# Performance work log

Measured on AMD Instinct MI355X. Metric: run time of the kernel, lower is better.

## Reference

```python
import jax, jax.numpy as jnp
import numpy as np

DIM = 96
HEADS = 6
WS = 8                      # window_size
OWS = int(WS * 0.5) + WS    # overlap_win_size = 12
PAD = (OWS - WS) // 2       # 2
Dd = Hh = Ww = 24
B = 1
L = Dd * Hh * Ww
MLP_H = DIM * 2
TBL = (WS + OWS - 1) ** 3   # 6859 relative-position-bias entries


def setup_inputs() -> dict:
    key = jax.random.key(0)
    ks = jax.random.split(key, 8)
    def n(k, shape, s=0.02):
        return jax.random.normal(k, shape, jnp.float32) * s
    return {
        "x": jax.random.normal(ks[0], (B, L, DIM), jnp.float32),
        "ln1_w": jnp.ones((DIM,), jnp.float32),
        "ln1_b": jnp.zeros((DIM,), jnp.float32),
        "qkv_w": n(ks[1], (3 * DIM, DIM)),
        "qkv_b": jnp.zeros((3 * DIM,), jnp.float32),
        "rpb": n(ks[2], (TBL, HEADS)),
        "proj_w": n(ks[3], (DIM, DIM)),
        "proj_b": jnp.zeros((DIM,), jnp.float32),
        "ln2_w": jnp.ones((DIM,), jnp.float32),
        "ln2_b": jnp.zeros((DIM,), jnp.float32),
        "fc1_w": n(ks[4], (MLP_H, DIM)),
        "fc1_b": jnp.zeros((MLP_H,), jnp.float32),
        "fc2_w": n(ks[5], (DIM, MLP_H)),
        "fc2_b": jnp.zeros((DIM,), jnp.float32),
        "rpi": jax.random.randint(ks[6], (WS ** 3, OWS ** 3), 0, TBL),
        "D": Dd, "H": Hh, "W": Ww,
    }


def _ln(x, w, b):
    m = jnp.mean(x, -1, keepdims=True)
    v = jnp.var(x, -1, keepdims=True)
    return (x - m) / jnp.sqrt(v + 1e-5) * w + b


def _ocab3d(x, ln1_w, ln1_b, qkv_w, qkv_b, rpb, proj_w, proj_b,
            ln2_w, ln2_b, fc1_w, fc1_b, fc2_w, fc2_b, rpi, D, H, W):
    Bz, Lz, C = x.shape
    hd = C // HEADS
    scale = hd ** -0.5
    shortcut = x

    xn = _ln(x, ln1_w, ln1_b).reshape(Bz, D, H, W, C)
    qkv = xn @ qkv_w.T + qkv_b                   # [B,D,H,W,3C]
    q = qkv[..., :C]
    kv = qkv[..., C:]                            # cat(k, v) on channels, [B,D,H,W,2C]

    nD, nH, nW = D // WS, H // WS, W // WS
    nw = nD * nH * nW

    # non-overlapping query windows -> [B*nw, WS^3, C]
    qw = q.reshape(Bz, nD, WS, nH, WS, nW, WS, C)
    qw = qw.transpose(0, 1, 3, 5, 2, 4, 6, 7).reshape(Bz * nw, WS ** 3, C)

    # overlapping kv windows via pad + strided gather (mirrors F.pad + unfold)
    kvp = jnp.pad(kv, ((0, 0), (PAD, PAD), (PAD, PAD), (PAD, PAD), (0, 0)))
    idx_d = (jnp.arange(nD) * WS)[:, None] + jnp.arange(OWS)[None, :]
    idx_h = (jnp.arange(nH) * WS)[:, None] + jnp.arange(OWS)[None, :]
    idx_w = (jnp.arange(nW) * WS)[:, None] + jnp.arange(OWS)[None, :]
    kw = kvp[:, idx_d]                 # [B,nD,OWS,Hp,Wp,2C]
    kw = kw[:, :, :, idx_h]            # [B,nD,OWS,nH,OWS,Wp,2C]
    kw = kw[:, :, :, :, :, idx_w]      # [B,nD,OWS,nH,OWS,nW,OWS,2C]
    kw = kw.transpose(0, 1, 3, 5, 2, 4, 6, 7).reshape(Bz * nw, OWS ** 3, 2 * C)
    kk, vv = kw[..., :C], kw[..., C:]

    qh = qw.reshape(-1, WS ** 3, HEADS, hd).transpose(0, 2, 1, 3) * scale
    kh = kk.reshape(-1, OWS ** 3, HEADS, hd).transpose(0, 2, 1, 3)
    vh = vv.reshape(-1, OWS ** 3, HEADS, hd).transpose(0, 2, 1, 3)

    attn = jnp.einsum('bhqd,bhkd->bhqk', qh, kh)               # [B*nw,H,512,1728]
    bias = rpb[rpi.reshape(-1)].reshape(WS ** 3, OWS ** 3, HEADS).transpose(2, 0, 1)
    attn = jax.nn.softmax(attn + bias[None], axis=-1)
    out = jnp.einsum('bhqk,bhkd->bhqd', attn, vh)
    out = out.transpose(0, 2, 1, 3).reshape(Bz * nw, WS ** 3, C)

    # window reverse -> [B, L, C]
    out = out.reshape(Bz, nD, nH, nW, WS, WS, WS, C)
    out = out.transpose(0, 1, 4, 2, 5, 3, 6, 7).reshape(Bz, D * H * W, C)

    x2 = out @ proj_w.T + proj_b + shortcut
    h1 = jax.nn.gelu(_ln(x2, ln2_w, ln2_b) @ fc1_w.T + fc1_b, approximate=False)
    return x2 + (h1 @ fc2_w.T + fc2_b)


def reference(x, ln1_w, ln1_b, qkv_w, qkv_b, rpb, proj_w, proj_b,
              ln2_w, ln2_b, fc1_w, fc1_b, fc2_w, fc2_b, rpi, D, H, W):
    return _ocab3d(x, ln1_w, ln1_b, qkv_w, qkv_b, rpb, proj_w, proj_b,
                   ln2_w, ln2_b, fc1_w, fc1_b, fc2_w, fc2_b, rpi, D, H, W)
```

## Files before the change

kernel.cpp:

```cpp
#include <hip/hip_runtime.h>
#include <math.h>

#define DIMC   96
#define NHEADS 6
#define HD     16
#define WSZ    8
#define OWSZ   12
#define PADW   2
#define DD     24
#define LTOK   13824
#define NWIN   27
#define NKEY   1728
#define NROW   512
#define MLPH   192
#define PDIM   28
#define PD3    21952
#define TBL    6859
#define LSTR   82944
#define AOSTR  1327104
#define LOG2E  1.4426950408889634f

typedef __attribute__((ext_vector_type(4))) short bf16x4;
typedef __attribute__((ext_vector_type(8))) short bf16x8;
typedef __attribute__((ext_vector_type(4))) float f32x4;

__device__ __forceinline__ unsigned short bfround(float f) {
    unsigned u = __float_as_uint(f);
    return (unsigned short)((u + 0x7FFFu + ((u >> 16) & 1u)) >> 16);
}
__device__ __forceinline__ unsigned bfpack(float a, float b) {
    unsigned ua = __float_as_uint(a), ub = __float_as_uint(b);
    ua = (ua + 0x7FFFu + ((ua >> 16) & 1u)) >> 16;
    ub = (ub + 0x7FFFu + ((ub >> 16) & 1u)) >> 16;
    return ua | (ub << 16);
}
__device__ __forceinline__ uint4 pack8(const float* v) {
    uint4 u;
    u.x = bfpack(v[0], v[1]); u.y = bfpack(v[2], v[3]);
    u.z = bfpack(v[4], v[5]); u.w = bfpack(v[6], v[7]);
    return u;
}
__device__ __forceinline__ bf16x4 pack4(f32x4 p) {
    union { uint2 u; bf16x4 v; } r;
    r.u.x = __builtin_amdgcn_perm(__float_as_uint(p[1]), __float_as_uint(p[0]), 0x07060302u);
    r.u.y = __builtin_amdgcn_perm(__float_as_uint(p[3]), __float_as_uint(p[2]), 0x07060302u);
    return r.v;
}
__device__ __forceinline__ f32x4 mfma16(bf16x4 a, bf16x4 b, f32x4 c) {
#if __has_builtin(__builtin_amdgcn_mfma_f32_16x16x16bf16_1k)
    return __builtin_amdgcn_mfma_f32_16x16x16bf16_1k(a, b, c, 0, 0, 0);
#else
    bf16x8 a8 = {a[0], a[1], a[2], a[3], 0, 0, 0, 0};
    bf16x8 b8 = {b[0], b[1], b[2], b[3], 0, 0, 0, 0};
    return __builtin_amdgcn_mfma_f32_16x16x32_bf16(a8, b8, c, 0, 0, 0);
#endif
}
__device__ __forceinline__ float fexp2(float x) {
#if __has_builtin(__builtin_amdgcn_exp2f)
    return __builtin_amdgcn_exp2f(x);
#else
    return exp2f(x);
#endif
}

#define QKVB 1296
#define ZB   515
#define WPB  45
#define BIASB 1296
__global__ __launch_bounds__(256) void qkvz_kernel(
        const float* __restrict__ X, const float* __restrict__ W,
        const float* __restrict__ bias, const float* __restrict__ lnw,
        const float* __restrict__ lnb,
        const float* __restrict__ projw, const float* __restrict__ fc1w,
        const float* __restrict__ fc2w,
        const int* __restrict__ rpi, const float* __restrict__ rpb,
        unsigned short* __restrict__ q16, unsigned short* __restrict__ kvp2,
        uint4* __restrict__ wpack, float* __restrict__ biasP) {
    __shared__ uint4 Af4[2 * 3 * 4 * 16];
    __shared__ uint4 Bf4[6 * 3 * 4 * 16];
    int bx = blockIdx.x, tid = threadIdx.x;

    if (bx >= QKVB + ZB + WPB) {
        int b2 = bx - (QKVB + ZB + WPB);
        int head = b2 / 216;
        int r2 = b2 % 216;
        int kt = r2 >> 1, qh = r2 & 1;
        int k0 = kt * 16;
        int qi = qh * 256 + tid;
        const int* rp = rpi + (long)qi * NKEY + k0;
        int idx[16];
        #pragma unroll
        for (int j = 0; j < 4; ++j) {
            int4 t = *(const int4*)(rp + j * 4);
            idx[j*4+0] = t.x; idx[j*4+1] = t.y; idx[j*4+2] = t.z; idx[j*4+3] = t.w;
        }
        #pragma unroll
        for (int quad = 0; quad < 4; ++quad) {
            float4 v;
            v.x = rpb[idx[quad*4+0] * NHEADS + head] * LOG2E;
            v.y = rpb[idx[quad*4+1] * NHEADS + head] * LOG2E;
            v.z = rpb[idx[quad*4+2] * NHEADS + head] * LOG2E;
            v.w = rpb[idx[quad*4+3] * NHEADS + head] * LOG2E;
            *(float4*)(biasP + ((((long)head*108 + kt)*4 + quad)*512 + qi)*4) = v;
        }
        return;
    }
    if (bx >= QKVB + ZB) {
        int u = (bx - QKVB - ZB) * 256 + tid;
        if (u < 5760) {
            int p = (u < 1152) ? u : (u < 3456 ? (u - 1152) % 1152 : (u - 3456) % 1152);
            int nn = p & 15, r = p >> 4, qg = r & 3, r2 = r >> 2;
            int kt = r2 % 3, ct = r2 / 3;
            int n = ct * 16 + nn, g = kt * 4 + qg;
            const float* src;
            if (u < 1152)      src = projw + n * 96 + g * 8;
            else if (u < 3456) { int nc = (u - 1152) / 1152; src = fc1w + (long)(nc * 96 + n) * 96 + g * 8; }
            else               { int kh = (u - 3456) / 1152; src = fc2w + (long)n * 192 + kh * 96 + g * 8; }
            const float4* s4 = (const float4*)src;
            float v[8];
            float4 t0 = s4[0], t1 = s4[1];
            v[0]=t0.x; v[1]=t0.y; v[2]=t0.z; v[3]=t0.w;
            v[4]=t1.x; v[5]=t1.y; v[6]=t1.z; v[7]=t1.w;
            wpack[u] = pack8(v);
        }
        return;
    }
    if (bx >= QKVB) {
        int t = (bx - QKVB) * 256 + tid;
        if (t < 21952 * 6) {
            int head = t / PD3, pos = t % PD3;
            int d = pos / 784, h = (pos / 28) % 28, w = pos % 28;
            if (d < 2 || d >= 26 || h < 2 || h >= 26 || w < 2 || w >= 26) {
                uint4* p = (uint4*)(kvp2 + ((long)head * PD3 + pos) * 32);
                uint4 z = make_uint4(0, 0, 0, 0);
                p[0] = z; p[1] = z; p[2] = z; p[3] = z;
            }
        }
        return;
    }

    int nc   = bx % 3;
    int row0 = (bx / 3) * 32;

    if (tid < 128) {
        int row = tid >> 2, part = tid & 3;
        int rt = row >> 4, mm = row & 15;
        float v[24];
        const float4* xp = (const float4*)(X + (long)(row0 + row) * 96 + part * 24);
        float s = 0.f, sq = 0.f;
        #pragma unroll
        for (int i = 0; i < 6; ++i) {
            float4 t = xp[i];
            v[i*4+0] = t.x; v[i*4+1] = t.y; v[i*4+2] = t.z; v[i*4+3] = t.w;
            s  += t.x + t.y + t.z + t.w;
            sq += t.x*t.x + t.y*t.y + t.z*t.z + t.w*t.w;
        }
        s  += __shfl_xor(s, 1);  s  += __shfl_xor(s, 2);
        sq += __shfl_xor(sq, 1); sq += __shfl_xor(sq, 2);
        float mean = s * (1.f / 96.f);
        float inv  = rsqrtf(sq * (1.f / 96.f) - mean * mean + 1e-5f);
        const float4* wp = (const float4*)(lnw + part * 24);
        const float4* bp = (const float4*)(lnb + part * 24);
        #pragma unroll
        for (int i = 0; i < 6; ++i) {
            float4 wv = wp[i], bv = bp[i];
            v[i*4+0] = (v[i*4+0] - mean) * inv * wv.x + bv.x;
            v[i*4+1] = (v[i*4+1] - mean) * inv * wv.y + bv.y;
            v[i*4+2] = (v[i*4+2] - mean) * inv * wv.z + bv.z;
            v[i*4+3] = (v[i*4+3] - mean) * inv * wv.w + bv.w;
        }
        #pragma unroll
        for (int gg = 0; gg < 3; ++gg) {
            int g = part * 3 + gg;
            int kt = g >> 2, qq = g & 3;
            Af4[((rt * 3 + kt) * 4 + qq) * 16 + mm] = pack8(v + gg * 8);
        }
    }
    for (int idx = tid; idx < 96 * 12; idx += 256) {
        int n = idx / 12;
        int g = idx % 12;
        const float4* wp = (const float4*)(W + (long)(nc * 96 + n) * 96 + g * 8);
        float v[8];
        float4 t0 = wp[0], t1 = wp[1];
        v[0]=t0.x; v[1]=t0.y; v[2]=t0.z; v[3]=t0.w;
        v[4]=t1.x; v[5]=t1.y; v[6]=t1.z; v[7]=t1.w;
        int ct = n >> 4, nn = n & 15, kt = g >> 2, qg = g & 3;
        Bf4[((ct * 3 + kt) * 4 + qg) * 16 + nn] = pack8(v);
    }
    __syncthreads();

    int wave = tid >> 6, lane = tid & 63;
    int qq = lane >> 4, mI = lane & 15;
    int rt = wave & 1, cg = wave >> 1;

    f32x4 acc[3];
    #pragma unroll
    for (int j = 0; j < 3; ++j) acc[j] = (f32x4){0.f, 0.f, 0.f, 0.f};
    #pragma unroll
    for (int kt = 0; kt < 3; ++kt) {
        bf16x8 a = *(const bf16x8*)&Af4[((rt * 3 + kt) * 4 + qq) * 16 + mI];
        #pragma unroll
        for (int j = 0; j < 3; ++j) {
            bf16x8 b = *(const bf16x8*)&Bf4[(((cg * 3 + j) * 3 + kt) * 4 + qq) * 16 + mI];
            acc[j] = __builtin_amdgcn_mfma_f32_16x16x32_bf16(a, b, acc[j], 0, 0, 0);
        }
    }

    float bv[3];
    #pragma unroll
    for (int j = 0; j < 3; ++j) bv[j] = bias[nc * 96 + (cg * 3 + j) * 16 + mI];
    #pragma unroll
    for (int r = 0; r < 4; ++r) {
        int row = row0 + rt * 16 + qq * 4 + r;
        if (nc == 0) {
            unsigned short* op = q16 + (long)row * 96;
            #pragma unroll
            for (int j = 0; j < 3; ++j)
                op[(cg * 3 + j) * 16 + mI] = bfround(0.25f * LOG2E * (acc[j][r] + bv[j]));
        } else {
            int d = row / 576, hh = (row / 24) % 24, w2 = row % 24;
            long pos = ((long)(d + 2) * 28 + (hh + 2)) * 28 + (w2 + 2);
            #pragma unroll
            for (int j = 0; j < 3; ++j) {
                int head = cg * 3 + j;
                kvp2[((long)head * PD3 + pos) * 32 +
                     (nc == 2 ? 16 : 0) + mI] = bfround(acc[j][r] + bv[j]);
            }
        }
    }
}

#define KSTR 20
#define VSTR 68
__global__ __launch_bounds__(256) void attn_kernel(
        const unsigned short* __restrict__ q, const unsigned short* __restrict__ kvp2,
        const float* __restrict__ biasP, float* __restrict__ ao,
        float* __restrict__ lbuf) {
    __shared__ unsigned short Ks[2][64 * KSTR];
    __shared__ unsigned short Vs[2][16 * VSTR];
    int bid = blockIdx.x;
    int w = bid / 48, rem = bid % 48;
    int head = rem >> 3;
    int quart = (rem >> 1) & 3, half = rem & 1;
    int wd8 = (w / 9) * 8, wh8 = ((w / 3) % 3) * 8, ww8 = (w % 3) * 8;
    int tid = threadIdx.x, wave = tid >> 6, lane = tid & 63;
    int quad = lane >> 4, m16 = lane & 15;
    int key = tid >> 2, part = tid & 3;
    int c0 = half ? 13 : 0;
    int cn = half ? 14 : 13;

    auto kvaddr = [&](int c) -> const uint4* {
        int jg = c * 64 + key;
        int i = jg / 144, jh = (jg / 12) % 12, jw = jg % 12;
        long sp = ((long)(wd8 + i) * PDIM + (wh8 + jh)) * PDIM + (ww8 + jw);
        return (const uint4*)(kvp2 + ((long)head * PD3 + sp) * 32 + part * 8);
    };
    auto writeLDS = [&](int b, uint4 v) {
        if (part < 2) {
            *(uint2*)(&Ks[b][key * KSTR + part * 8])     = make_uint2(v.x, v.y);
            *(uint2*)(&Ks[b][key * KSTR + part * 8 + 4]) = make_uint2(v.z, v.w);
        } else {
            int d0 = (part - 2) * 8;
            Vs[b][(d0+0)*VSTR + key] = (unsigned short)(v.x);
            Vs[b][(d0+1)*VSTR + key] = (unsigned short)(v.x >> 16);
            Vs[b][(d0+2)*VSTR + key] = (unsigned short)(v.y);
            Vs[b][(d0+3)*VSTR + key] = (unsigned short)(v.y >> 16);
            Vs[b][(d0+4)*VSTR + key] = (unsigned short)(v.z);
            Vs[b][(d0+5)*VSTR + key] = (unsigned short)(v.z >> 16);
            Vs[b][(d0+6)*VSTR + key] = (unsigned short)(v.w);
            Vs[b][(d0+7)*VSTR + key] = (unsigned short)(v.w >> 16);
        }
    };

    int grow[2]; bf16x4 qf[2];
    #pragma unroll
    for (int qt = 0; qt < 2; ++qt) {
        int ql = quart * 128 + wave * 32 + qt * 16 + m16;
        int ld = ql >> 6, lh = (ql >> 3) & 7, lw = ql & 7;
        grow[qt] = ((wd8 + ld) * 24 + (wh8 + lh)) * 24 + (ww8 + lw);
        qf[qt] = *(const bf16x4*)(q + (long)grow[qt] * 96 + head * 16 + quad * 4);
    }

    const float* bbase = biasP + (long)head * 884736 + quad * 2048
                         + ((quart * 128 + wave * 32 + m16) << 2);
    f32x4 bcur[2][4];
    #pragma unroll
    for (int qt = 0; qt < 2; ++qt)
        #pragma unroll
        for (int kt = 0; kt < 4; ++kt)
            bcur[qt][kt] = *(const f32x4*)(bbase + (long)(c0*4 + kt) * 8192 + qt * 64);

    writeLDS(0, *kvaddr(c0));

    const bf16x4 onesf = {(short)0x3F80, (short)0x3F80, (short)0x3F80, (short)0x3F80};
    f32x4 o[2], lacc[2];
    o[0] = (f32x4){0.f,0.f,0.f,0.f}; o[1] = (f32x4){0.f,0.f,0.f,0.f};
    lacc[0] = o[0]; lacc[1] = o[1];
    uint4 stgn;

    #pragma unroll 1
    for (int cc = 0; cc < cn; ++cc) {
        int c = c0 + cc;
        if (cc + 1 < cn) stgn = *kvaddr(c + 1);
        __syncthreads();
        int b = cc & 1;

        bf16x4 kf[4];
        #pragma unroll
        for (int kt = 0; kt < 4; ++kt)
            kf[kt] = *(const bf16x4*)(&Ks[b][(kt * 16 + m16) * KSTR + quad * 4]);

        f32x4 S[2][4];
        #pragma unroll
        for (int qt = 0; qt < 2; ++qt)
            #pragma unroll
            for (int kt = 0; kt < 4; ++kt)
                S[qt][kt] = mfma16(kf[kt], qf[qt], bcur[qt][kt]);

        if (cc + 1 < cn) {
            const float* bp = bbase + (long)(c + 1) * 32768;
            #pragma unroll
            for (int qt = 0; qt < 2; ++qt)
                #pragma unroll
                for (int kt = 0; kt < 4; ++kt)
                    bcur[qt][kt] = *(const f32x4*)(bp + kt * 8192 + qt * 64);
        }

        bf16x4 Pb[2][4];
        #pragma unroll
        for (int qt = 0; qt < 2; ++qt)
            #pragma unroll
            for (int kt = 0; kt < 4; ++kt) {
                f32x4 p;
                #pragma unroll
                for (int r = 0; r < 4; ++r) p[r] = fexp2(S[qt][kt][r]);
                Pb[qt][kt] = pack4(p);
                lacc[qt] = mfma16(onesf, Pb[qt][kt], lacc[qt]);
            }

        #pragma unroll
        for (int kt = 0; kt < 4; ++kt) {
            bf16x4 vf = *(const bf16x4*)(&Vs[b][m16 * VSTR + kt * 16 + quad * 4]);
            o[0] = mfma16(vf, Pb[0][kt], o[0]);
            o[1] = mfma16(vf, Pb[1][kt], o[1]);
        }

        if (cc + 1 < cn) writeLDS((cc + 1) & 1, stgn);
    }

    float* aout = ao + (long)half * AOSTR;
    float* lout = lbuf + (long)half * LSTR;
    #pragma unroll
    for (int qt = 0; qt < 2; ++qt) {
        float4* op = (float4*)(aout + (long)grow[qt] * 96 + head * 16 + quad * 4);
        *op = make_float4(o[qt][0], o[qt][1], o[qt][2], o[qt][3]);
        if (quad == 0) lout[grow[qt] * 6 + head] = lacc[qt][0];
    }
}

#define X2S 100
__global__ __launch_bounds__(512) void mlp_kernel(
        const float* __restrict__ ao0, const float* __restrict__ ao1,
        const float* __restrict__ lbuf, const uint4* __restrict__ wpack,
        const float* __restrict__ projb, const float* __restrict__ x,
        const float* __restrict__ ln2w, const float* __restrict__ ln2b,
        const float* __restrict__ fc1b, const float* __restrict__ fc2b,
        float* __restrict__ out) {
    __shared__ uint4 Ws[5760];
    __shared__ uint4 Af4[4 * 3 * 4 * 16];
    __shared__ float x2s[64 * X2S];
    __shared__ unsigned short h16[64 * 192];
    int tid = threadIdx.x;
    int row0 = blockIdx.x * 64;
    int wave = tid >> 6, lane = tid & 63;
    int qq = lane >> 4, mI = lane & 15;
    int rt = wave & 3, cg = wave >> 2;

    for (int idx = tid; idx < 5760; idx += 512) Ws[idx] = wpack[idx];

    if (tid < 256) {
        int row = tid >> 2, part = tid & 3;
        int rtA = row >> 4, mm = row & 15;
        int grow = row0 + row;
        const float4* a0 = (const float4*)(ao0 + (long)grow * 96 + part * 24);
        const float4* a1 = (const float4*)(ao1 + (long)grow * 96 + part * 24);
        int ha = (part * 3) >> 1, hb = ha + 1;
        float inva = 1.f / (lbuf[grow*6 + ha] + lbuf[LSTR + grow*6 + ha]);
        float invb = 1.f / (lbuf[grow*6 + hb] + lbuf[LSTR + grow*6 + hb]);
        float v[24];
        #pragma unroll
        for (int i = 0; i < 6; ++i) {
            float4 u0 = a0[i], u1 = a1[i];
            #pragma unroll
            for (int j = 0; j < 4; ++j) {
                int gc = part * 24 + i * 4 + j;
                float lv = ((gc >> 4) == ha) ? inva : invb;
                float s = (j==0?u0.x+u1.x : j==1?u0.y+u1.y : j==2?u0.z+u1.z : u0.w+u1.w);
                v[i*4+j] = s * lv;
            }
        }
        #pragma unroll
        for (int gg = 0; gg < 3; ++gg) {
            int g = part * 3 + gg;
            int kt = g >> 2, q4 = g & 3;
            Af4[((rtA * 3 + kt) * 4 + q4) * 16 + mm] = pack8(v + gg * 8);
        }
    }
    __syncthreads();

    {
        f32x4 acc[3];
        #pragma unroll
        for (int j = 0; j < 3; ++j) acc[j] = (f32x4){0.f,0.f,0.f,0.f};
        #pragma unroll
        for (int kt = 0; kt < 3; ++kt) {
            bf16x8 a = *(const bf16x8*)&Af4[((rt * 3 + kt) * 4 + qq) * 16 + mI];
            #pragma unroll
            for (int j = 0; j < 3; ++j) {
                bf16x8 b = *(const bf16x8*)&Ws[(((cg * 3 + j) * 3 + kt) * 4 + qq) * 16 + mI];
                acc[j] = __builtin_amdgcn_mfma_f32_16x16x32_bf16(a, b, acc[j], 0, 0, 0);
            }
        }
        float bv[3];
        #pragma unroll
        for (int j = 0; j < 3; ++j) bv[j] = projb[(cg * 3 + j) * 16 + mI];
        #pragma unroll
        for (int r = 0; r < 4; ++r) {
            int row = rt * 16 + qq * 4 + r;
            int grow = row0 + row;
            #pragma unroll
            for (int j = 0; j < 3; ++j) {
                int col = (cg * 3 + j) * 16 + mI;
                x2s[row * X2S + col] = acc[j][r] + bv[j] + x[(long)grow * 96 + col];
            }
        }
    }
    __syncthreads();

    if (tid < 256) {
        int row = tid >> 2, part = tid & 3;
        int rtA = row >> 4, mm = row & 15;
        float v[24];
        const float4* xp = (const float4*)(x2s + row * X2S + part * 24);
        float s = 0.f, sq = 0.f;
        #pragma unroll
        for (int i = 0; i < 6; ++i) {
            float4 t = xp[i];
            v[i*4+0] = t.x; v[i*4+1] = t.y; v[i*4+2] = t.z; v[i*4+3] = t.w;
            s  += t.x + t.y + t.z + t.w;
            sq += t.x*t.x + t.y*t.y + t.z*t.z + t.w*t.w;
        }
        s  += __shfl_xor(s, 1);  s  += __shfl_xor(s, 2);
        sq += __shfl_xor(sq, 1); sq += __shfl_xor(sq, 2);
        float mean = s * (1.f / 96.f);
        float inv  = rsqrtf(sq * (1.f / 96.f) - mean * mean + 1e-5f);
        const float4* wp = (const float4*)(ln2w + part * 24);
        const float4* bp = (const float4*)(ln2b + part * 24);
        #pragma unroll
        for (int i = 0; i < 6; ++i) {
            float4 wv = wp[i], bv = bp[i];
            v[i*4+0] = (v[i*4+0] - mean) * inv * wv.x + bv.x;
            v[i*4+1] = (v[i*4+1] - mean) * inv * wv.y + bv.y;
            v[i*4+2] = (v[i*4+2] - mean) * inv * wv.z + bv.z;
            v[i*4+3] = (v[i*4+3] - mean) * inv * wv.w + bv.w;
        }
        #pragma unroll
        for (int gg = 0; gg < 3; ++gg) {
            int g = part * 3 + gg;
            int kt = g >> 2, q4 = g & 3;
            Af4[((rtA * 3 + kt) * 4 + q4) * 16 + mm] = pack8(v + gg * 8);
        }
    }
    __syncthreads();

    #pragma unroll
    for (int nc = 0; nc < 2; ++nc) {
        f32x4 acc[3];
        #pragma unroll
        for (int j = 0; j < 3; ++j) acc[j] = (f32x4){0.f,0.f,0.f,0.f};
        #pragma unroll
        for (int kt = 0; kt < 3; ++kt) {
            bf16x8 a = *(const bf16x8*)&Af4[((rt * 3 + kt) * 4 + qq) * 16 + mI];
            #pragma unroll
            for (int j = 0; j < 3; ++j) {
                bf16x8 b = *(const bf16x8*)&Ws[1152 + nc * 1152 +
                               (((cg * 3 + j) * 3 + kt) * 4 + qq) * 16 + mI];
                acc[j] = __builtin_amdgcn_mfma_f32_16x16x32_bf16(a, b, acc[j], 0, 0, 0);
            }
        }
        float bv[3];
        #pragma unroll
        for (int j = 0; j < 3; ++j) bv[j] = fc1b[nc * 96 + (cg * 3 + j) * 16 + mI];
        #pragma unroll
        for (int r = 0; r < 4; ++r) {
            int row = rt * 16 + qq * 4 + r;
            #pragma unroll
            for (int j = 0; j < 3; ++j) {
                int col = nc * 96 + (cg * 3 + j) * 16 + mI;
                float v = acc[j][r] + bv[j];
                float g = 0.5f * v * (1.f + erff(v * 0.70710678f));
                int fi = (((row >> 4) * 6 + (col >> 5)) * 4 + ((col >> 3) & 3)) * 16 + (row & 15);
                h16[fi * 8 + (col & 7)] = bfround(g);
            }
        }
    }
    __syncthreads();

    f32x4 acc2[3];
    #pragma unroll
    for (int j = 0; j < 3; ++j) acc2[j] = (f32x4){0.f,0.f,0.f,0.f};
    #pragma unroll
    for (int kh = 0; kh < 2; ++kh) {
        #pragma unroll
        for (int kt = 0; kt < 3; ++kt) {
            int ktA = kh * 3 + kt;
            bf16x8 a = *(const bf16x8*)&h16[(((rt * 6 + ktA) * 4 + qq) * 16 + mI) * 8];
            #pragma unroll
            for (int j = 0; j < 3; ++j) {
                bf16x8 b = *(const bf16x8*)&Ws[3456 + kh * 1152 +
                               (((cg * 3 + j) * 3 + kt) * 4 + qq) * 16 + mI];
                acc2[j] = __builtin_amdgcn_mfma_f32_16x16x32_bf16(a, b, acc2[j], 0, 0, 0);
            }
        }
    }
    float bv[3];
    #pragma unroll
    for (int j = 0; j < 3; ++j) bv[j] = fc2b[(cg * 3 + j) * 16 + mI];
    #pragma unroll
    for (int r = 0; r < 4; ++r) {
        int row = rt * 16 + qq * 4 + r;
        int grow = row0 + row;
        #pragma unroll
        for (int j = 0; j < 3; ++j) {
            int col = (cg * 3 + j) * 16 + mI;
            out[(long)grow * 96 + col] = acc2[j][r] + bv[j] + x2s[row * X2S + col];
        }
    }
}

extern "C" void kernel_launch(void* const* d_in, const int* in_sizes, int n_in,
                              void* d_out, int out_size, void* d_ws, size_t ws_size,
                              hipStream_t stream) {
    const float* x     = (const float*)d_in[0];
    const float* ln1w  = (const float*)d_in[1];
    const float* ln1b  = (const float*)d_in[2];
    const float* qkvw  = (const float*)d_in[3];
    const float* qkvb  = (const float*)d_in[4];
    const float* rpb   = (const float*)d_in[5];
    const float* projw = (const float*)d_in[6];
    const float* projb = (const float*)d_in[7];
    const float* ln2w  = (const float*)d_in[8];
    const float* ln2b  = (const float*)d_in[9];
    const float* fc1w  = (const float*)d_in[10];
    const float* fc1b  = (const float*)d_in[11];
    const float* fc2w  = (const float*)d_in[12];
    const float* fc2b  = (const float*)d_in[13];
    const int*   rpi   = (const int*)d_in[14];
    float* outp = (float*)d_out;

    float* ws = (float*)d_ws;
    float*          aop    = ws;
    unsigned short* q16    = (unsigned short*)(ws + 2654208);
    unsigned short* kvp16  = (unsigned short*)(ws + 3317760);
    float*          biasPf = ws + 5425152;
    float*          lbuf   = ws + 10733568;
    uint4*          wpack  = (uint4*)(ws + 10899456);

    qkvz_kernel<<<QKVB + ZB + WPB + BIASB, 256, 0, stream>>>(
        x, qkvw, qkvb, ln1w, ln1b, projw, fc1w, fc2w, rpi, rpb,
        q16, kvp16, wpack, biasPf);
    attn_kernel<<<NWIN * NHEADS * 4 * 2, 256, 0, stream>>>(q16, kvp16, biasPf, aop, lbuf);
    mlp_kernel<<<LTOK / 64, 512, 0, stream>>>(aop, aop + AOSTR, lbuf, wpack, projb, x,
                                              ln2w, ln2b, fc1b, fc2b, outp);
}
```

Before: 179.7 us.

## Share rpi gather across heads and transpose MFMA operand order in attention

The bias-prep blocks now loop over all six heads per block, so each rpi index tile is loaded once instead of six times, and the block count drops from 1296 to 216. In the attention kernel V is stored key-major with vector writes instead of eight scalar transposed stores, and the MFMA operands are swapped so P is the A operand. The output tile therefore comes out transposed, giving scalar per-element stores to ao and lbuf. The next-chunk bias is loaded into a separate register set, which raises register pressure.

```diff
diff --git a/kernel.cpp b/kernel.cpp
--- a/kernel.cpp
+++ b/kernel.cpp
@@ -66,7 +66,7 @@
 #define QKVB 1296
 #define ZB   515
 #define WPB  45
-#define BIASB 1296
+#define BIASB 216
 __global__ __launch_bounds__(256) void qkvz_kernel(
         const float* __restrict__ X, const float* __restrict__ W,
         const float* __restrict__ bias, const float* __restrict__ lnw,
@@ -82,9 +82,7 @@
 
     if (bx >= QKVB + ZB + WPB) {
         int b2 = bx - (QKVB + ZB + WPB);
-        int head = b2 / 216;
-        int r2 = b2 % 216;
-        int kt = r2 >> 1, qh = r2 & 1;
+        int kt = b2 >> 1, qh = b2 & 1;
         int k0 = kt * 16;
         int qi = qh * 256 + tid;
         const int* rp = rpi + (long)qi * NKEY + k0;
@@ -92,16 +90,20 @@
         #pragma unroll
         for (int j = 0; j < 4; ++j) {
             int4 t = *(const int4*)(rp + j * 4);
-            idx[j*4+0] = t.x; idx[j*4+1] = t.y; idx[j*4+2] = t.z; idx[j*4+3] = t.w;
-        }
-        #pragma unroll
-        for (int quad = 0; quad < 4; ++quad) {
-            float4 v;
-            v.x = rpb[idx[quad*4+0] * NHEADS + head] * LOG2E;
-            v.y = rpb[idx[quad*4+1] * NHEADS + head] * LOG2E;
-            v.z = rpb[idx[quad*4+2] * NHEADS + head] * LOG2E;
-            v.w = rpb[idx[quad*4+3] * NHEADS + head] * LOG2E;
-            *(float4*)(biasP + ((((long)head*108 + kt)*4 + quad)*512 + qi)*4) = v;
+            idx[j*4+0] = t.x * NHEADS; idx[j*4+1] = t.y * NHEADS;
+            idx[j*4+2] = t.z * NHEADS; idx[j*4+3] = t.w * NHEADS;
+        }
+        #pragma unroll
+        for (int head = 0; head < NHEADS; ++head) {
+            #pragma unroll
+            for (int quad = 0; quad < 4; ++quad) {
+                float4 v;
+                v.x = rpb[idx[quad*4+0] + head] * LOG2E;
+                v.y = rpb[idx[quad*4+1] + head] * LOG2E;
+                v.z = rpb[idx[quad*4+2] + head] * LOG2E;
+                v.w = rpb[idx[quad*4+3] + head] * LOG2E;
+                *(float4*)(biasP + ((((long)head*108 + kt)*4 + quad)*512 + qi)*4) = v;
+            }
         }
         return;
     }
@@ -231,13 +233,13 @@
 }
 
 #define KSTR 20
-#define VSTR 68
+#define VST2 22
 __global__ __launch_bounds__(256) void attn_kernel(
         const unsigned short* __restrict__ q, const unsigned short* __restrict__ kvp2,
         const float* __restrict__ biasP, float* __restrict__ ao,
         float* __restrict__ lbuf) {
     __shared__ unsigned short Ks[2][64 * KSTR];
-    __shared__ unsigned short Vs[2][16 * VSTR];
+    __shared__ unsigned short Vs[2][64 * VST2];
     int bid = blockIdx.x;
     int w = bid / 48, rem = bid % 48;
     int head = rem >> 3;
@@ -261,24 +263,18 @@
             *(uint2*)(&Ks[b][key * KSTR + part * 8 + 4]) = make_uint2(v.z, v.w);
         } else {
             int d0 = (part - 2) * 8;
-            Vs[b][(d0+0)*VSTR + key] = (unsigned short)(v.x);
-            Vs[b][(d0+1)*VSTR + key] = (unsigned short)(v.x >> 16);
-            Vs[b][(d0+2)*VSTR + key] = (unsigned short)(v.y);
-            Vs[b][(d0+3)*VSTR + key] = (unsigned short)(v.y >> 16);
-            Vs[b][(d0+4)*VSTR + key] = (unsigned short)(v.z);
-            Vs[b][(d0+5)*VSTR + key] = (unsigned short)(v.z >> 16);
-            Vs[b][(d0+6)*VSTR + key] = (unsigned short)(v.w);
-            Vs[b][(d0+7)*VSTR + key] = (unsigned short)(v.w >> 16);
+            *(uint2*)(&Vs[b][key * VST2 + d0])     = make_uint2(v.x, v.y);
+            *(uint2*)(&Vs[b][key * VST2 + d0 + 4]) = make_uint2(v.z, v.w);
         }
     };
 
-    int grow[2]; bf16x4 qf[2];
+    bf16x4 qf[2];
     #pragma unroll
     for (int qt = 0; qt < 2; ++qt) {
         int ql = quart * 128 + wave * 32 + qt * 16 + m16;
         int ld = ql >> 6, lh = (ql >> 3) & 7, lw = ql & 7;
-        grow[qt] = ((wd8 + ld) * 24 + (wh8 + lh)) * 24 + (ww8 + lw);
-        qf[qt] = *(const bf16x4*)(q + (long)grow[qt] * 96 + head * 16 + quad * 4);
+        int g = ((wd8 + ld) * 24 + (wh8 + lh)) * 24 + (ww8 + lw);
+        qf[qt] = *(const bf16x4*)(q + (long)g * 96 + head * 16 + quad * 4);
     }
 
     const float* bbase = biasP + (long)head * 884736 + quad * 2048
@@ -317,13 +313,14 @@
             for (int kt = 0; kt < 4; ++kt)
                 S[qt][kt] = mfma16(kf[kt], qf[qt], bcur[qt][kt]);
 
+        f32x4 bnxt[2][4];
         if (cc + 1 < cn) {
             const float* bp = bbase + (long)(c + 1) * 32768;
             #pragma unroll
             for (int qt = 0; qt < 2; ++qt)
                 #pragma unroll
                 for (int kt = 0; kt < 4; ++kt)
-                    bcur[qt][kt] = *(const f32x4*)(bp + kt * 8192 + qt * 64);
+                    bnxt[qt][kt] = *(const f32x4*)(bp + kt * 8192 + qt * 64);
         }
 
         bf16x4 Pb[2][4];
@@ -335,26 +332,40 @@
                 #pragma unroll
                 for (int r = 0; r < 4; ++r) p[r] = fexp2(S[qt][kt][r]);
                 Pb[qt][kt] = pack4(p);
-                lacc[qt] = mfma16(onesf, Pb[qt][kt], lacc[qt]);
+                lacc[qt] = mfma16(Pb[qt][kt], onesf, lacc[qt]);
             }
 
         #pragma unroll
         for (int kt = 0; kt < 4; ++kt) {
-            bf16x4 vf = *(const bf16x4*)(&Vs[b][m16 * VSTR + kt * 16 + quad * 4]);
-            o[0] = mfma16(vf, Pb[0][kt], o[0]);
-            o[1] = mfma16(vf, Pb[1][kt], o[1]);
+            union { unsigned short s[4]; bf16x4 v; } u;
+            int base = (kt * 16 + quad * 4) * VST2 + m16;
+            u.s[0] = Vs[b][base];
+            u.s[1] = Vs[b][base + VST2];
+            u.s[2] = Vs[b][base + 2 * VST2];
+            u.s[3] = Vs[b][base + 3 * VST2];
+            o[0] = mfma16(Pb[0][kt], u.v, o[0]);
+            o[1] = mfma16(Pb[1][kt], u.v, o[1]);
         }
 
         if (cc + 1 < cn) writeLDS((cc + 1) & 1, stgn);
+        #pragma unroll
+        for (int qt = 0; qt < 2; ++qt)
+            #pragma unroll
+            for (int kt = 0; kt < 4; ++kt) bcur[qt][kt] = bnxt[qt][kt];
     }
 
     float* aout = ao + (long)half * AOSTR;
     float* lout = lbuf + (long)half * LSTR;
     #pragma unroll
     for (int qt = 0; qt < 2; ++qt) {
-        float4* op = (float4*)(aout + (long)grow[qt] * 96 + head * 16 + quad * 4);
-        *op = make_float4(o[qt][0], o[qt][1], o[qt][2], o[qt][3]);
-        if (quad == 0) lout[grow[qt] * 6 + head] = lacc[qt][0];
+        #pragma unroll
+        for (int r = 0; r < 4; ++r) {
+            int ql = quart * 128 + wave * 32 + qt * 16 + quad * 4 + r;
+            int ld = ql >> 6, lh = (ql >> 3) & 7, lw = ql & 7;
+            int g = ((wd8 + ld) * 24 + (wh8 + lh)) * 24 + (ww8 + lw);
+            aout[(long)g * 96 + head * 16 + m16] = o[qt][r];
+            if (m16 == 0) lout[g * 6 + head] = lacc[qt][r];
+        }
     }
 }
 
```

Measured after the change: 170.2 us. 1.06x faster.
